# Kernel tuning notes

Hardware: AMD Instinct MI355X
Metric: run time of the kernel (lower is better)

## Reference

```python
import jax, jax.numpy as jnp
import numpy as np

N_NODES = 50000


def _graph_conv(x, src, dst, W, b):
    """DGL GraphConv with norm='both', bias, weight applied pre-aggregation.
    x: [N, Fin]; src/dst: [E] int; W: [Fin, Fout]; b: [Fout]."""
    N = x.shape[0]
    ones = jnp.ones(src.shape, jnp.float32)
    deg_out = jnp.maximum(jax.ops.segment_sum(ones, src, num_segments=N), 1.0)
    deg_in = jnp.maximum(jax.ops.segment_sum(ones, dst, num_segments=N), 1.0)
    h = (x * jax.lax.rsqrt(deg_out)[:, None]) @ W          # [N, Fout]
    m = jax.ops.segment_sum(h[src], dst, num_segments=N)   # SpMM aggregate
    return m * jax.lax.rsqrt(deg_in)[:, None] + b


def setup_inputs() -> dict:
    key = jax.random.key(0)
    ks = jax.random.split(key, 12)
    N = N_NODES
    e_sizes = {"rsr": 3000000, "rtr": 1000000, "rur": 200000}
    inp = {"x": jax.random.normal(ks[0], (N, 32), jnp.float32)}
    for i, (name, E) in enumerate(e_sizes.items()):
        inp[f"src_{name}"] = jax.random.randint(ks[1 + 2 * i], (E,), 0, N, jnp.int64)
        inp[f"dst_{name}"] = jax.random.randint(ks[2 + 2 * i], (E,), 0, N, jnp.int64)
    inp["W1"] = jax.random.normal(ks[7], (3, 32, 16), jnp.float32) / np.sqrt(32.0)
    inp["b1"] = jnp.zeros((3, 16), jnp.float32)
    inp["W2"] = jax.random.normal(ks[8], (3, 16, 1), jnp.float32) / np.sqrt(16.0)
    inp["b2"] = jnp.zeros((3, 1), jnp.float32)
    return inp


def reference(x, src_rsr, dst_rsr, src_rtr, dst_rtr, src_rur, dst_rur, W1, b1, W2, b2):
    edges = [(src_rsr, dst_rsr), (src_rtr, dst_rtr), (src_rur, dst_rur)]
    # layer 1: HeteroGraphConv(sum over relations) -> relu
    h = sum(_graph_conv(x, s, d, W1[r], b1[r]) for r, (s, d) in enumerate(edges))
    h = jax.nn.relu(h)
    # layer 2 -> squeeze
    out = sum(_graph_conv(h, s, d, W2[r], b2[r]) for r, (s, d) in enumerate(edges))
    return out[:, 0]
```

## Files before the change

kernel.cpp:

```cpp
#include <hip/hip_runtime.h>

#define N_NODES 50000
#define FH 16
#define NBUK 782
#define BSHIFT 6
#define BSTRIDE 800
#define TILE 4096
#define NCH2 64
#define NRNG 8
#define RNGSZ 6250
#define C1CAP 4608

#define OFF_INVOUT   0u
#define OFF_INVIN    150000u
#define OFF_BUKCNT   300000u
#define OFF_BSTART   302400u
#define OFF_GCUR     304800u
#define OFF_ROWPTR   307200u
#define OFF_HPROJ    457216u
#define OFF_AGGP     3657216u
#define OFF_SRCHIST  3657216u
#define OFF_HS       6057216u
#define OFF_PAIRS    6357216u
#define OFF_SRCSORT  10557216u

__global__ __launch_bounds__(256) void k_srcDeg(const int* s0, const int* s1, const int* s2,
                                                int E0, int E1, int E2,
                                                unsigned* __restrict__ histP,
                                                unsigned* __restrict__ bukCnt) {
    __shared__ unsigned bins[RNGSZ / 2];
    int c = blockIdx.x, rg = blockIdx.y, r = blockIdx.z;
    if (c == 0 && rg == 0 && r == 0) {
        for (int i = threadIdx.x; i < 3 * BSTRIDE; i += 256) bukCnt[i] = 0u;
    }
    const int* arr = (r == 0) ? s0 : (r == 1) ? s1 : s2;
    int E = (r == 0) ? E0 : (r == 1) ? E1 : E2;
    for (int i = threadIdx.x; i < RNGSZ / 2; i += 256) bins[i] = 0u;
    __syncthreads();
    int lo = rg * RNGSZ;
    int per = (((E + NCH2 - 1) / NCH2) + 7) & ~7;
    int a0 = c * per, a1 = min(a0 + per, E);
    for (int i = a0 + (int)threadIdx.x * 8; i < a1; i += 2048) {
        if (i + 8 <= a1) {
            int4 v1 = *reinterpret_cast<const int4*>(arr + i);
            int4 v2 = *reinterpret_cast<const int4*>(arr + i + 4);
            unsigned d0 = (unsigned)(v1.x - lo), d1 = (unsigned)(v1.y - lo);
            unsigned d2 = (unsigned)(v1.z - lo), d3 = (unsigned)(v1.w - lo);
            unsigned d4 = (unsigned)(v2.x - lo), d5 = (unsigned)(v2.y - lo);
            unsigned d6 = (unsigned)(v2.z - lo), d7 = (unsigned)(v2.w - lo);
            if (d0 < (unsigned)RNGSZ) atomicAdd(&bins[d0 >> 1], (d0 & 1u) ? 65536u : 1u);
            if (d1 < (unsigned)RNGSZ) atomicAdd(&bins[d1 >> 1], (d1 & 1u) ? 65536u : 1u);
            if (d2 < (unsigned)RNGSZ) atomicAdd(&bins[d2 >> 1], (d2 & 1u) ? 65536u : 1u);
            if (d3 < (unsigned)RNGSZ) atomicAdd(&bins[d3 >> 1], (d3 & 1u) ? 65536u : 1u);
            if (d4 < (unsigned)RNGSZ) atomicAdd(&bins[d4 >> 1], (d4 & 1u) ? 65536u : 1u);
            if (d5 < (unsigned)RNGSZ) atomicAdd(&bins[d5 >> 1], (d5 & 1u) ? 65536u : 1u);
            if (d6 < (unsigned)RNGSZ) atomicAdd(&bins[d6 >> 1], (d6 & 1u) ? 65536u : 1u);
            if (d7 < (unsigned)RNGSZ) atomicAdd(&bins[d7 >> 1], (d7 & 1u) ? 65536u : 1u);
        } else {
            for (int k2 = i; k2 < a1; k2++) {
                unsigned d = (unsigned)(arr[k2] - lo);
                if (d < (unsigned)RNGSZ) atomicAdd(&bins[d >> 1], (d & 1u) ? 65536u : 1u);
            }
        }
    }
    __syncthreads();
    unsigned* out = histP + ((size_t)r * NCH2 + c) * 25000 + rg * (RNGSZ / 2);
    for (int i = threadIdx.x; i < RNGSZ / 2; i += 256) out[i] = bins[i];
}

__global__ __launch_bounds__(256) void k_misc(const unsigned* __restrict__ histP,
                                              float* __restrict__ invOut,
                                              const int* d0p, const int* d1p, const int* d2p,
                                              int E0, int E1, int E2,
                                              unsigned* __restrict__ bukCnt) {
    __shared__ unsigned bins[NBUK];
    int r = blockIdx.y;
    if (blockIdx.x < 196) {
        int n = blockIdx.x * 256 + threadIdx.x;
        if (n >= N_NODES) return;
        const unsigned* p = histP + (size_t)r * NCH2 * 25000 + (n >> 1);
        unsigned s = 0;
#pragma unroll
        for (int c = 0; c < NCH2; c++) {
            unsigned w = p[(size_t)c * 25000];
            s += (n & 1) ? (w >> 16) : (w & 0xFFFFu);
        }
        invOut[r * N_NODES + n] = rsqrtf((float)(s ? s : 1u));
        return;
    }
    int c = blockIdx.x - 196;
    const int* arr = (r == 0) ? d0p : (r == 1) ? d1p : d2p;
    int E = (r == 0) ? E0 : (r == 1) ? E1 : E2;
    for (int i = threadIdx.x; i < NBUK; i += 256) bins[i] = 0u;
    __syncthreads();
    int per = (((E + 255) / 256) + 3) & ~3;
    int a0 = c * per, a1 = min(a0 + per, E);
    for (int i = a0 + (int)threadIdx.x * 4; i < a1; i += 1024) {
        if (i + 4 <= a1) {
            int4 v = *reinterpret_cast<const int4*>(arr + i);
            atomicAdd(&bins[((unsigned)v.x) >> BSHIFT], 1u);
            atomicAdd(&bins[((unsigned)v.y) >> BSHIFT], 1u);
            atomicAdd(&bins[((unsigned)v.z) >> BSHIFT], 1u);
            atomicAdd(&bins[((unsigned)v.w) >> BSHIFT], 1u);
        } else {
            for (int k2 = i; k2 < a1; k2++)
                atomicAdd(&bins[((unsigned)arr[k2]) >> BSHIFT], 1u);
        }
    }
    __syncthreads();
    for (int b = threadIdx.x; b < NBUK; b += 256)
        if (bins[b]) atomicAdd(&bukCnt[r * BSTRIDE + b], bins[b]);
}

__global__ __launch_bounds__(256) void k_bucketScan(const unsigned* __restrict__ bukCnt,
                                                    unsigned* __restrict__ bstart,
                                                    unsigned* __restrict__ gcur) {
    __shared__ unsigned part[256];
    int r = blockIdx.x, t = threadIdx.x;
    unsigned loc[4]; unsigned s = 0;
#pragma unroll
    for (int k = 0; k < 4; k++) {
        int idx = 4 * t + k;
        loc[k] = (idx < NBUK) ? bukCnt[r * BSTRIDE + idx] : 0u;
        s += loc[k];
    }
    part[t] = s;
    __syncthreads();
    for (int d = 1; d < 256; d <<= 1) {
        unsigned v = (t >= d) ? part[t - d] : 0u;
        __syncthreads();
        part[t] += v;
        __syncthreads();
    }
    unsigned run = part[t] - s;
#pragma unroll
    for (int k = 0; k < 4; k++) {
        int idx = 4 * t + k;
        if (idx <= NBUK) { bstart[r * BSTRIDE + idx] = run; gcur[r * BSTRIDE + idx] = run; }
        run += loc[k];
    }
}

__global__ __launch_bounds__(256) void k_passB(
    const int* s0p, const int* s1p, const int* s2p,
    const int* d0p, const int* d1p, const int* d2p,
    int E0, int E1, int E2, int po0, int po1, int po2,
    unsigned* __restrict__ pairsAll, unsigned* __restrict__ gcurAll) {
    __shared__ unsigned cnt[NBUK];
    __shared__ unsigned off[NBUK];
    __shared__ unsigned gbase[NBUK];
    __shared__ unsigned part[256];
    __shared__ unsigned spair[TILE];
    __shared__ unsigned saddr[TILE];
    int r = blockIdx.z;
    const int* src = (r == 0) ? s0p : (r == 1) ? s1p : s2p;
    const int* dst = (r == 0) ? d0p : (r == 1) ? d1p : d2p;
    int E = (r == 0) ? E0 : (r == 1) ? E1 : E2;
    unsigned* pairs = pairsAll + ((r == 0) ? po0 : (r == 1) ? po1 : po2);
    unsigned* gcur = gcurAll + r * BSTRIDE;
    int nb = gridDim.x;
    int chunk = (((E + nb - 1) / nb) + 15) & ~15;
    int c0 = blockIdx.x * chunk;
    int c1 = min(c0 + chunk, E);
    for (int t0 = c0; t0 < c1; t0 += TILE) {
        int tn = min(TILE, c1 - t0);
        for (int i = threadIdx.x; i < NBUK; i += 256) cnt[i] = 0u;
        __syncthreads();
        unsigned pk[16], bk[16], sl[16];
        if (tn == TILE) {
            int base = t0 + (int)threadIdx.x * 16;
#pragma unroll
            for (int q = 0; q < 4; q++) {
                int4 vs = *reinterpret_cast<const int4*>(src + base + q * 4);
                int4 vd = *reinterpret_cast<const int4*>(dst + base + q * 4);
                pk[q * 4 + 0] = ((unsigned)vd.x << 16) | (unsigned)vs.x;
                pk[q * 4 + 1] = ((unsigned)vd.y << 16) | (unsigned)vs.y;
                pk[q * 4 + 2] = ((unsigned)vd.z << 16) | (unsigned)vs.z;
                pk[q * 4 + 3] = ((unsigned)vd.w << 16) | (unsigned)vs.w;
                bk[q * 4 + 0] = (unsigned)vd.x >> BSHIFT;
                bk[q * 4 + 1] = (unsigned)vd.y >> BSHIFT;
                bk[q * 4 + 2] = (unsigned)vd.z >> BSHIFT;
                bk[q * 4 + 3] = (unsigned)vd.w >> BSHIFT;
            }
#pragma unroll
            for (int k = 0; k < 16; k++) sl[k] = atomicAdd(&cnt[bk[k]], 1u);
        } else {
#pragma unroll
            for (int k = 0; k < 16; k++) {
                int ii = k * 256 + (int)threadIdx.x;
                bk[k] = 0xFFFFFFFFu;
                if (ii < tn) {
                    int i = t0 + ii;
                    unsigned s = (unsigned)src[i], d = (unsigned)dst[i];
                    pk[k] = (d << 16) | s;
                    unsigned b = d >> BSHIFT;
                    bk[k] = b;
                    sl[k] = atomicAdd(&cnt[b], 1u);
                }
            }
        }
        __syncthreads();
        {
            int t = threadIdx.x;
            unsigned loc[4]; unsigned sloc = 0;
#pragma unroll
            for (int k2 = 0; k2 < 4; k2++) {
                int idx = 4 * t + k2;
                loc[k2] = (idx < NBUK) ? cnt[idx] : 0u;
                sloc += loc[k2];
            }
            part[t] = sloc;
            __syncthreads();
            for (int d = 1; d < 256; d <<= 1) {
                unsigned v = (t >= d) ? part[t - d] : 0u;
                __syncthreads();
                part[t] += v;
                __syncthreads();
            }
            unsigned run = part[t] - sloc;
#pragma unroll
            for (int k2 = 0; k2 < 4; k2++) {
                int idx = 4 * t + k2;
                if (idx < NBUK) off[idx] = run;
                run += loc[k2];
            }
        }
        __syncthreads();
        for (int b = threadIdx.x; b < NBUK; b += 256) {
            unsigned c = cnt[b];
            if (c) gbase[b] = atomicAdd(&gcur[b], c);
        }
        __syncthreads();
        if (tn == TILE) {
#pragma unroll
            for (int k = 0; k < 16; k++) {
                unsigned idx = off[bk[k]] + sl[k];
                spair[idx] = pk[k];
                saddr[idx] = gbase[bk[k]] + sl[k];
            }
        } else {
#pragma unroll
            for (int k = 0; k < 16; k++) {
                if (bk[k] != 0xFFFFFFFFu) {
                    unsigned idx = off[bk[k]] + sl[k];
                    spair[idx] = pk[k];
                    saddr[idx] = gbase[bk[k]] + sl[k];
                }
            }
        }
        __syncthreads();
#pragma unroll
        for (int k = 0; k < 16; k++) {
            int ii = k * 256 + (int)threadIdx.x;
            if (ii < tn) pairs[saddr[ii]] = spair[ii];
        }
        __syncthreads();
    }
}

__global__ __launch_bounds__(256) void k_h1(const float* __restrict__ x, const float* __restrict__ invOut,
                                            const float* __restrict__ W1, float* __restrict__ hproj) {
    __shared__ float sW[32 * FH];
    __shared__ float sx[16][32];
    int r = blockIdx.y;
    const float* W = W1 + r * 32 * FH;
    int t = threadIdx.x;
    for (int i = t; i < 32 * FH; i += 256) sW[i] = W[i];
    int n0 = blockIdx.x * 16;
    for (int i = t; i < 16 * 32; i += 256) {
        int nn = i >> 5, kk = i & 31;
        int n = n0 + nn;
        sx[nn][kk] = (n < N_NODES) ? x[n * 32 + kk] : 0.0f;
    }
    __syncthreads();
    int nn = t >> 4, j = t & 15;
    int n = n0 + nn;
    if (n < N_NODES) {
        float s = 0.f;
#pragma unroll
        for (int k = 0; k < 32; k++) s += sx[nn][k] * sW[k * FH + j];
        hproj[((size_t)r * N_NODES + n) * FH + j] = s * invOut[r * N_NODES + n];
    }
}

__global__ __launch_bounds__(256) void k_passC1(
    const unsigned* __restrict__ pairsAll, int po1, int po2,
    const unsigned* __restrict__ bstartAll,
    const float4* __restrict__ h4All, float4* __restrict__ out4All,
    unsigned short* __restrict__ srcGAll, unsigned* __restrict__ rowptrAll,
    float* __restrict__ invInAll) {
    __shared__ unsigned cnt[64];
    __shared__ unsigned off[65];
    __shared__ unsigned cur[64];
    __shared__ unsigned short srcS[C1CAP];
    int b = blockIdx.x, t = threadIdx.x, r = blockIdx.z;
    int po = (r == 0) ? 0 : (r == 1) ? po1 : po2;
    const unsigned* pairs = pairsAll + po;
    const unsigned* bstart = bstartAll + r * BSTRIDE;
    const float4* h4 = h4All + (size_t)r * N_NODES * 4;
    float4* out4 = out4All + (size_t)r * N_NODES * 4;
    unsigned short* srcG = srcGAll + po;
    unsigned* rowptr = rowptrAll + (size_t)r * (N_NODES + 1);
    float* invIn = invInAll + (size_t)r * N_NODES;
    unsigned e0 = bstart[b], e1 = bstart[b + 1];
    if (e1 - e0 > (unsigned)C1CAP) e1 = e0 + (unsigned)C1CAP;
    int d0 = b << BSHIFT;
    if (t < 64) cnt[t] = 0u;
    __syncthreads();
    for (unsigned i = e0 + t; i < e1; i += 256)
        atomicAdd(&cnt[(pairs[i] >> 16) - (unsigned)d0], 1u);
    __syncthreads();
    if (t < 64) {
        unsigned cv = cnt[t];
        unsigned sc = cv;
#pragma unroll
        for (int d = 1; d < 64; d <<= 1) {
            unsigned v = __shfl_up(sc, d, 64);
            if (t >= d) sc += v;
        }
        off[t] = sc - cv;
        if (t == 63) off[64] = sc;
    }
    __syncthreads();
    if (t < 64) {
        cur[t] = off[t];
        int n = d0 + t;
        if (n < N_NODES) {
            rowptr[n] = (unsigned)po + e0 + off[t];
            unsigned dg = cnt[t];
            invIn[n] = rsqrtf((float)(dg ? dg : 1u));
        }
    }
    if (b == NBUK - 1 && t == 0) rowptr[N_NODES] = (unsigned)po + e1;
    __syncthreads();
    for (unsigned i = e0 + t; i < e1; i += 256) {
        unsigned p = pairs[i];
        unsigned d = (p >> 16) - (unsigned)d0;
        unsigned pos = atomicAdd(&cur[d], 1u);
        srcS[pos] = (unsigned short)(p & 0xFFFFu);
    }
    __syncthreads();
    {
        unsigned len = e1 - e0;
        for (unsigned i = t; i < len; i += 256) srcG[e0 + i] = srcS[i];
    }
    int unit = t >> 4, p = t & 15, k = p >> 2, fq = p & 3;
    for (int nd = unit; nd < 64; nd += 16) {
        unsigned o0 = off[nd], o1 = off[nd + 1];
        float ax = 0.f, ay = 0.f, az = 0.f, aw = 0.f;
        unsigned base = o0;
        for (; base + 8 <= o1; base += 8) {
            int s0 = srcS[base + k], s1 = srcS[base + 4 + k];
            float4 v0 = h4[(size_t)s0 * 4 + fq];
            float4 v1 = h4[(size_t)s1 * 4 + fq];
            ax += v0.x + v1.x; ay += v0.y + v1.y; az += v0.z + v1.z; aw += v0.w + v1.w;
        }
        for (; base < o1; base += 4) {
            unsigned idx = base + (unsigned)k;
            if (idx < o1) {
                int s = srcS[idx];
                float4 v = h4[(size_t)s * 4 + fq];
                ax += v.x; ay += v.y; az += v.z; aw += v.w;
            }
        }
        ax += __shfl_xor(ax, 4, 16); ay += __shfl_xor(ay, 4, 16);
        az += __shfl_xor(az, 4, 16); aw += __shfl_xor(aw, 4, 16);
        ax += __shfl_xor(ax, 8, 16); ay += __shfl_xor(ay, 8, 16);
        az += __shfl_xor(az, 8, 16); aw += __shfl_xor(aw, 8, 16);
        int n = d0 + nd;
        if (k == 0 && n < N_NODES) {
            unsigned dg = o1 - o0;
            float sc = rsqrtf((float)(dg ? dg : 1u));
            float4 res; res.x = ax * sc; res.y = ay * sc; res.z = az * sc; res.w = aw * sc;
            out4[(size_t)n * 4 + fq] = res;
        }
    }
}

__global__ __launch_bounds__(256) void k_relu_h2(const float4* __restrict__ aggP4,
                                                 const float* __restrict__ invOut,
                                                 const float* __restrict__ b1,
                                                 const float* __restrict__ W2,
                                                 float* __restrict__ hs) {
    __shared__ float sW[3 * FH];
    __shared__ float sb[FH];
    int t = threadIdx.x;
    if (t < 48) sW[t] = W2[t];
    if (t < 16) sb[t] = b1[t] + b1[FH + t] + b1[2 * FH + t];
    __syncthreads();
    int n = blockIdx.x * 256 + t;
    if (n >= N_NODES) return;
    const size_t SL4 = (size_t)N_NODES * 4;
    float h[FH];
#pragma unroll
    for (int q = 0; q < 4; q++) {
        float4 a0 = aggP4[(size_t)n * 4 + q];
        float4 a1 = aggP4[SL4 + (size_t)n * 4 + q];
        float4 a2 = aggP4[2 * SL4 + (size_t)n * 4 + q];
        h[q * 4 + 0] = fmaxf(a0.x + a1.x + a2.x + sb[q * 4 + 0], 0.f);
        h[q * 4 + 1] = fmaxf(a0.y + a1.y + a2.y + sb[q * 4 + 1], 0.f);
        h[q * 4 + 2] = fmaxf(a0.z + a1.z + a2.z + sb[q * 4 + 2], 0.f);
        h[q * 4 + 3] = fmaxf(a0.w + a1.w + a2.w + sb[q * 4 + 3], 0.f);
    }
#pragma unroll
    for (int r = 0; r < 3; r++) {
        float s = 0.f;
#pragma unroll
        for (int j = 0; j < FH; j++) s += h[j] * sW[r * FH + j];
        hs[r * N_NODES + n] = s * invOut[r * N_NODES + n];
    }
}

__global__ __launch_bounds__(256) void k_passC2f(
    const unsigned short* __restrict__ srcG, const unsigned* __restrict__ rowptr,
    const float* __restrict__ hsAll, const float* __restrict__ invIn,
    const float* __restrict__ b2, float* __restrict__ out) {
    int t = threadIdx.x;
    int unit = t >> 4, p = t & 15;
    int n = blockIdx.x * 16 + unit;
    if (n >= N_NODES) return;
    float tot = 0.f;
#pragma unroll
    for (int r = 0; r < 3; r++) {
        unsigned o0 = rowptr[r * (N_NODES + 1) + n];
        unsigned o1 = rowptr[r * (N_NODES + 1) + n + 1];
        const float* hs = hsAll + (size_t)r * N_NODES;
        float s = 0.f;
        for (unsigned i = o0 + (unsigned)p; i < o1; i += 16) s += hs[srcG[i]];
        tot += s * invIn[r * N_NODES + n];
    }
    tot += __shfl_xor(tot, 1, 16); tot += __shfl_xor(tot, 2, 16);
    tot += __shfl_xor(tot, 4, 16); tot += __shfl_xor(tot, 8, 16);
    if (p == 0) out[n] = tot + b2[0] + b2[1] + b2[2];
}


__global__ void f_zero(float* __restrict__ p, int n) {
    int i = blockIdx.x * blockDim.x + threadIdx.x;
    if (i < n) p[i] = 0.0f;
}
__global__ void f_deg(const int* __restrict__ src, const int* __restrict__ dst, int E,
                      float* __restrict__ dout, float* __restrict__ din) {
    int i = blockIdx.x * blockDim.x + threadIdx.x;
    if (i < E) { atomicAdd(&dout[src[i]], 1.0f); atomicAdd(&din[dst[i]], 1.0f); }
}
__global__ void f_rsqrt(float* __restrict__ p, int n) {
    int i = blockIdx.x * blockDim.x + threadIdx.x;
    if (i < n) p[i] = rsqrtf(fmaxf(p[i], 1.0f));
}
__global__ void f_agg1(const int* __restrict__ src, const int* __restrict__ dst, int E,
                       const float* __restrict__ h, const float* __restrict__ invin,
                       float* __restrict__ agg) {
    int idx = blockIdx.x * blockDim.x + threadIdx.x;
    if (idx < E * FH) {
        int e = idx >> 4, j = idx & 15;
        atomicAdd(&agg[dst[e] * FH + j], h[src[e] * FH + j] * invin[dst[e]]);
    }
}
__global__ void f_relu(float* __restrict__ agg, const float* __restrict__ b1) {
    int i = blockIdx.x * blockDim.x + threadIdx.x;
    if (i < N_NODES * FH) {
        int j = i & 15;
        agg[i] = fmaxf(agg[i] + b1[j] + b1[FH + j] + b1[2 * FH + j], 0.0f);
    }
}
__global__ void f_outinit(float* __restrict__ out, const float* __restrict__ b2) {
    int i = blockIdx.x * blockDim.x + threadIdx.x;
    if (i < N_NODES) out[i] = b2[0] + b2[1] + b2[2];
}
__global__ void f_h2(const float* __restrict__ h1, const float* __restrict__ invout,
                     const float* __restrict__ W2r, float* __restrict__ hsv) {
    int n = blockIdx.x * blockDim.x + threadIdx.x;
    if (n < N_NODES) {
        const float4* hp = (const float4*)(h1 + (size_t)n * FH);
        float s = 0.0f;
#pragma unroll
        for (int q = 0; q < 4; q++) {
            float4 hv = hp[q];
            s += hv.x * W2r[q * 4] + hv.y * W2r[q * 4 + 1] + hv.z * W2r[q * 4 + 2] + hv.w * W2r[q * 4 + 3];
        }
        hsv[n] = s * invout[n];
    }
}
__global__ void f_agg2(const int* __restrict__ src, const int* __restrict__ dst, int E,
                       const float* __restrict__ hsv, const float* __restrict__ invin,
                       float* __restrict__ out) {
    int e = blockIdx.x * blockDim.x + threadIdx.x;
    if (e < E) atomicAdd(&out[dst[e]], hsv[src[e]] * invin[dst[e]]);
}


extern "C" void kernel_launch(void* const* d_in, const int* in_sizes, int n_in,
                              void* d_out, int out_size, void* d_ws, size_t ws_size,
                              hipStream_t stream) {
    const float* x = (const float*)d_in[0];
    const int* srcs[3] = { (const int*)d_in[1], (const int*)d_in[3], (const int*)d_in[5] };
    const int* dsts[3] = { (const int*)d_in[2], (const int*)d_in[4], (const int*)d_in[6] };
    int E[3] = { in_sizes[1], in_sizes[3], in_sizes[5] };
    const float* W1 = (const float*)d_in[7];
    const float* b1 = (const float*)d_in[8];
    const float* W2 = (const float*)d_in[9];
    const float* b2 = (const float*)d_in[10];
    float* out = (float*)d_out;
    const int N = N_NODES;
    const int B = 256;
    size_t Etot = (size_t)E[0] + E[1] + E[2];
    size_t need = ((size_t)OFF_SRCSORT + (Etot + 1) / 2) * 4u;

    if (ws_size >= need) {
        unsigned* ws = (unsigned*)d_ws;
        float* invOut = (float*)(ws + OFF_INVOUT);
        float* invIn  = (float*)(ws + OFF_INVIN);
        unsigned* bukCnt = ws + OFF_BUKCNT;
        unsigned* bstart = ws + OFF_BSTART;
        unsigned* gcur   = ws + OFF_GCUR;
        unsigned* rowptr = ws + OFF_ROWPTR;
        float* hproj = (float*)(ws + OFF_HPROJ);
        float* aggP  = (float*)(ws + OFF_AGGP);
        unsigned* srcHist = ws + OFF_SRCHIST;
        float* hs    = (float*)(ws + OFF_HS);
        unsigned* pairs = ws + OFF_PAIRS;
        unsigned short* srcSort = (unsigned short*)(ws + OFF_SRCSORT);
        int po[3] = { 0, E[0], E[0] + E[1] };

        k_srcDeg<<<dim3(NCH2, NRNG, 3), B, 0, stream>>>(srcs[0], srcs[1], srcs[2],
                                                        E[0], E[1], E[2], srcHist, bukCnt);
        k_misc<<<dim3(196 + 256, 3), B, 0, stream>>>(srcHist, invOut,
                                                     dsts[0], dsts[1], dsts[2],
                                                     E[0], E[1], E[2], bukCnt);
        k_bucketScan<<<3, B, 0, stream>>>(bukCnt, bstart, gcur);
        k_passB<<<dim3(256, 1, 3), B, 0, stream>>>(
            srcs[0], srcs[1], srcs[2], dsts[0], dsts[1], dsts[2],
            E[0], E[1], E[2], po[0], po[1], po[2], pairs, gcur);
        k_h1<<<dim3((N + 15) / 16, 3), B, 0, stream>>>(x, invOut, W1, hproj);
        k_passC1<<<dim3(NBUK, 1, 3), B, 0, stream>>>(
            pairs, po[1], po[2], bstart,
            (const float4*)hproj, (float4*)aggP,
            srcSort, rowptr, invIn);
        k_relu_h2<<<(N + B - 1) / B, B, 0, stream>>>((const float4*)aggP, invOut, b1, W2, hs);
        k_passC2f<<<(N + 15) / 16, B, 0, stream>>>(srcSort, rowptr, hs, invIn, b2, out);
    } else {
        float* wsf = (float*)d_ws;
        float* invOut = wsf;
        float* invIn = wsf + 3 * (size_t)N;
        float* h = wsf + 6 * (size_t)N;
        float* agg = wsf + 22 * (size_t)N;
        float* hsv = wsf + 38 * (size_t)N;
        f_zero<<<(6 * N + B - 1) / B, B, 0, stream>>>(invOut, 6 * N);
        f_zero<<<(16 * N + B - 1) / B, B, 0, stream>>>(agg, 16 * N);
        for (int r = 0; r < 3; r++)
            f_deg<<<(E[r] + B - 1) / B, B, 0, stream>>>(srcs[r], dsts[r], E[r],
                                                        invOut + (size_t)r * N, invIn + (size_t)r * N);
        f_rsqrt<<<(6 * N + B - 1) / B, B, 0, stream>>>(invOut, 6 * N);
        for (int r = 0; r < 3; r++) {
            k_h1<<<dim3((N + 15) / 16, 1), B, 0, stream>>>(x, invOut + (size_t)r * N,
                                                           W1 + (size_t)r * 32 * FH, h);
            f_agg1<<<(E[r] * FH + B - 1) / B, B, 0, stream>>>(srcs[r], dsts[r], E[r], h,
                                                              invIn + (size_t)r * N, agg);
        }
        f_relu<<<(N * FH + B - 1) / B, B, 0, stream>>>(agg, b1);
        f_outinit<<<(N + B - 1) / B, B, 0, stream>>>(out, b2);
        for (int r = 0; r < 3; r++) {
            f_h2<<<(N + B - 1) / B, B, 0, stream>>>(agg, invOut + (size_t)r * N,
                                                    W2 + (size_t)r * FH, hsv);
            f_agg2<<<(E[r] + B - 1) / B, B, 0, stream>>>(srcs[r], dsts[r], E[r], hsv,
                                                         invIn + (size_t)r * N, out);
        }
    }
}
```

Before: 242.6 us.

## Merge preprocessing kernels to cut launches and drop global bucket atomics

Fuses the source-degree and destination-bucket histograms into one launch, writing per-chunk bucket counts instead of using global atomics. Degree reduction and the bucket scan share one kernel that sums the partial counts. The partition pass and the layer-1 projection share a launch as disjoint block ranges. Together these go from six launches to three and let independent work fill the GPU together. The cost is extra partial-count memory and a serial 32-way sum per bucket in the scan block.

Result: slower. 247.7 us (+2.1%).

```diff
diff --git a/kernel.cpp b/kernel.cpp
--- a/kernel.cpp
+++ b/kernel.cpp
@@ -9,91 +9,73 @@
 #define NCH2 64
 #define NRNG 8
 #define RNGSZ 6250
+#define NDCH 32
 #define C1CAP 4608
 
 #define OFF_INVOUT   0u
 #define OFF_INVIN    150000u
-#define OFF_BUKCNT   300000u
 #define OFF_BSTART   302400u
 #define OFF_GCUR     304800u
 #define OFF_ROWPTR   307200u
 #define OFF_HPROJ    457216u
 #define OFF_AGGP     3657216u
 #define OFF_SRCHIST  3657216u
+#define OFF_BUKCNTP  8457216u
 #define OFF_HS       6057216u
 #define OFF_PAIRS    6357216u
 #define OFF_SRCSORT  10557216u
 
-__global__ __launch_bounds__(256) void k_srcDeg(const int* s0, const int* s1, const int* s2,
-                                                int E0, int E1, int E2,
-                                                unsigned* __restrict__ histP,
-                                                unsigned* __restrict__ bukCnt) {
+__global__ __launch_bounds__(256) void k_hist(
+    const int* s0, const int* s1, const int* s2,
+    const int* d0p, const int* d1p, const int* d2p,
+    int E0, int E1, int E2,
+    unsigned* __restrict__ histP, unsigned* __restrict__ bukCntP) {
     __shared__ unsigned bins[RNGSZ / 2];
-    int c = blockIdx.x, rg = blockIdx.y, r = blockIdx.z;
-    if (c == 0 && rg == 0 && r == 0) {
-        for (int i = threadIdx.x; i < 3 * BSTRIDE; i += 256) bukCnt[i] = 0u;
-    }
-    const int* arr = (r == 0) ? s0 : (r == 1) ? s1 : s2;
-    int E = (r == 0) ? E0 : (r == 1) ? E1 : E2;
-    for (int i = threadIdx.x; i < RNGSZ / 2; i += 256) bins[i] = 0u;
-    __syncthreads();
-    int lo = rg * RNGSZ;
-    int per = (((E + NCH2 - 1) / NCH2) + 7) & ~7;
-    int a0 = c * per, a1 = min(a0 + per, E);
-    for (int i = a0 + (int)threadIdx.x * 8; i < a1; i += 2048) {
-        if (i + 8 <= a1) {
-            int4 v1 = *reinterpret_cast<const int4*>(arr + i);
-            int4 v2 = *reinterpret_cast<const int4*>(arr + i + 4);
-            unsigned d0 = (unsigned)(v1.x - lo), d1 = (unsigned)(v1.y - lo);
-            unsigned d2 = (unsigned)(v1.z - lo), d3 = (unsigned)(v1.w - lo);
-            unsigned d4 = (unsigned)(v2.x - lo), d5 = (unsigned)(v2.y - lo);
-            unsigned d6 = (unsigned)(v2.z - lo), d7 = (unsigned)(v2.w - lo);
-            if (d0 < (unsigned)RNGSZ) atomicAdd(&bins[d0 >> 1], (d0 & 1u) ? 65536u : 1u);
-            if (d1 < (unsigned)RNGSZ) atomicAdd(&bins[d1 >> 1], (d1 & 1u) ? 65536u : 1u);
-            if (d2 < (unsigned)RNGSZ) atomicAdd(&bins[d2 >> 1], (d2 & 1u) ? 65536u : 1u);
-            if (d3 < (unsigned)RNGSZ) atomicAdd(&bins[d3 >> 1], (d3 & 1u) ? 65536u : 1u);
-            if (d4 < (unsigned)RNGSZ) atomicAdd(&bins[d4 >> 1], (d4 & 1u) ? 65536u : 1u);
-            if (d5 < (unsigned)RNGSZ) atomicAdd(&bins[d5 >> 1], (d5 & 1u) ? 65536u : 1u);
-            if (d6 < (unsigned)RNGSZ) atomicAdd(&bins[d6 >> 1], (d6 & 1u) ? 65536u : 1u);
-            if (d7 < (unsigned)RNGSZ) atomicAdd(&bins[d7 >> 1], (d7 & 1u) ? 65536u : 1u);
-        } else {
-            for (int k2 = i; k2 < a1; k2++) {
-                unsigned d = (unsigned)(arr[k2] - lo);
-                if (d < (unsigned)RNGSZ) atomicAdd(&bins[d >> 1], (d & 1u) ? 65536u : 1u);
-            }
-        }
-    }
-    __syncthreads();
-    unsigned* out = histP + ((size_t)r * NCH2 + c) * 25000 + rg * (RNGSZ / 2);
-    for (int i = threadIdx.x; i < RNGSZ / 2; i += 256) out[i] = bins[i];
-}
-
-__global__ __launch_bounds__(256) void k_misc(const unsigned* __restrict__ histP,
-                                              float* __restrict__ invOut,
-                                              const int* d0p, const int* d1p, const int* d2p,
-                                              int E0, int E1, int E2,
-                                              unsigned* __restrict__ bukCnt) {
-    __shared__ unsigned bins[NBUK];
-    int r = blockIdx.y;
-    if (blockIdx.x < 196) {
-        int n = blockIdx.x * 256 + threadIdx.x;
-        if (n >= N_NODES) return;
-        const unsigned* p = histP + (size_t)r * NCH2 * 25000 + (n >> 1);
-        unsigned s = 0;
-#pragma unroll
-        for (int c = 0; c < NCH2; c++) {
-            unsigned w = p[(size_t)c * 25000];
-            s += (n & 1) ? (w >> 16) : (w & 0xFFFFu);
-        }
-        invOut[r * N_NODES + n] = rsqrtf((float)(s ? s : 1u));
+    int bx = blockIdx.x;
+    if (bx < NCH2 * NRNG * 3) {
+        int c = bx % NCH2, rg = (bx / NCH2) % NRNG, r = bx / (NCH2 * NRNG);
+        const int* arr = (r == 0) ? s0 : (r == 1) ? s1 : s2;
+        int E = (r == 0) ? E0 : (r == 1) ? E1 : E2;
+        for (int i = threadIdx.x; i < RNGSZ / 2; i += 256) bins[i] = 0u;
+        __syncthreads();
+        int lo = rg * RNGSZ;
+        int per = (((E + NCH2 - 1) / NCH2) + 7) & ~7;
+        int a0 = c * per, a1 = min(a0 + per, E);
+        for (int i = a0 + (int)threadIdx.x * 8; i < a1; i += 2048) {
+            if (i + 8 <= a1) {
+                int4 v1 = *reinterpret_cast<const int4*>(arr + i);
+                int4 v2 = *reinterpret_cast<const int4*>(arr + i + 4);
+                unsigned d0 = (unsigned)(v1.x - lo), d1 = (unsigned)(v1.y - lo);
+                unsigned d2 = (unsigned)(v1.z - lo), d3 = (unsigned)(v1.w - lo);
+                unsigned d4 = (unsigned)(v2.x - lo), d5 = (unsigned)(v2.y - lo);
+                unsigned d6 = (unsigned)(v2.z - lo), d7 = (unsigned)(v2.w - lo);
+                if (d0 < (unsigned)RNGSZ) atomicAdd(&bins[d0 >> 1], (d0 & 1u) ? 65536u : 1u);
+                if (d1 < (unsigned)RNGSZ) atomicAdd(&bins[d1 >> 1], (d1 & 1u) ? 65536u : 1u);
+                if (d2 < (unsigned)RNGSZ) atomicAdd(&bins[d2 >> 1], (d2 & 1u) ? 65536u : 1u);
+                if (d3 < (unsigned)RNGSZ) atomicAdd(&bins[d3 >> 1], (d3 & 1u) ? 65536u : 1u);
+                if (d4 < (unsigned)RNGSZ) atomicAdd(&bins[d4 >> 1], (d4 & 1u) ? 65536u : 1u);
+                if (d5 < (unsigned)RNGSZ) atomicAdd(&bins[d5 >> 1], (d5 & 1u) ? 65536u : 1u);
+                if (d6 < (unsigned)RNGSZ) atomicAdd(&bins[d6 >> 1], (d6 & 1u) ? 65536u : 1u);
+                if (d7 < (unsigned)RNGSZ) atomicAdd(&bins[d7 >> 1], (d7 & 1u) ? 65536u : 1u);
+            } else {
+                for (int k2 = i; k2 < a1; k2++) {
+                    unsigned d = (unsigned)(arr[k2] - lo);
+                    if (d < (unsigned)RNGSZ) atomicAdd(&bins[d >> 1], (d & 1u) ? 65536u : 1u);
+                }
+            }
+        }
+        __syncthreads();
+        unsigned* out = histP + ((size_t)r * NCH2 + c) * 25000 + rg * (RNGSZ / 2);
+        for (int i = threadIdx.x; i < RNGSZ / 2; i += 256) out[i] = bins[i];
         return;
     }
-    int c = blockIdx.x - 196;
+    int idx = bx - NCH2 * NRNG * 3;
+    int c = idx % NDCH, r = idx / NDCH;
     const int* arr = (r == 0) ? d0p : (r == 1) ? d1p : d2p;
     int E = (r == 0) ? E0 : (r == 1) ? E1 : E2;
     for (int i = threadIdx.x; i < NBUK; i += 256) bins[i] = 0u;
     __syncthreads();
-    int per = (((E + 255) / 256) + 3) & ~3;
+    int per = (((E + NDCH - 1) / NDCH) + 3) & ~3;
     int a0 = c * per, a1 = min(a0 + per, E);
     for (int i = a0 + (int)threadIdx.x * 4; i < a1; i += 1024) {
         if (i + 4 <= a1) {
@@ -108,21 +90,41 @@
         }
     }
     __syncthreads();
-    for (int b = threadIdx.x; b < NBUK; b += 256)
-        if (bins[b]) atomicAdd(&bukCnt[r * BSTRIDE + b], bins[b]);
-}
-
-__global__ __launch_bounds__(256) void k_bucketScan(const unsigned* __restrict__ bukCnt,
-                                                    unsigned* __restrict__ bstart,
-                                                    unsigned* __restrict__ gcur) {
+    unsigned* outp = bukCntP + ((size_t)r * NDCH + c) * BSTRIDE;
+    for (int b = threadIdx.x; b < NBUK; b += 256) outp[b] = bins[b];
+}
+
+__global__ __launch_bounds__(256) void k_prep(const unsigned* __restrict__ histP,
+                                              float* __restrict__ invOut,
+                                              const unsigned* __restrict__ bukCntP,
+                                              unsigned* __restrict__ bstart,
+                                              unsigned* __restrict__ gcur) {
+    int r = blockIdx.y;
+    if (blockIdx.x < 196) {
+        int n = blockIdx.x * 256 + threadIdx.x;
+        if (n >= N_NODES) return;
+        const unsigned* p = histP + (size_t)r * NCH2 * 25000 + (n >> 1);
+        unsigned s = 0;
+#pragma unroll
+        for (int c = 0; c < NCH2; c++) {
+            unsigned w = p[(size_t)c * 25000];
+            s += (n & 1) ? (w >> 16) : (w & 0xFFFFu);
+        }
+        invOut[r * N_NODES + n] = rsqrtf((float)(s ? s : 1u));
+        return;
+    }
     __shared__ unsigned part[256];
-    int r = blockIdx.x, t = threadIdx.x;
+    int t = threadIdx.x;
     unsigned loc[4]; unsigned s = 0;
 #pragma unroll
     for (int k = 0; k < 4; k++) {
         int idx = 4 * t + k;
-        loc[k] = (idx < NBUK) ? bukCnt[r * BSTRIDE + idx] : 0u;
-        s += loc[k];
+        unsigned v = 0;
+        if (idx < NBUK) {
+            const unsigned* p = bukCntP + (size_t)r * NDCH * BSTRIDE + idx;
+            for (int c = 0; c < NDCH; c++) v += p[(size_t)c * BSTRIDE];
+        }
+        loc[k] = v; s += v;
     }
     part[t] = s;
     __syncthreads();
@@ -141,26 +143,55 @@
     }
 }
 
-__global__ __launch_bounds__(256) void k_passB(
+__global__ __launch_bounds__(256) void k_passB_h1(
     const int* s0p, const int* s1p, const int* s2p,
     const int* d0p, const int* d1p, const int* d2p,
     int E0, int E1, int E2, int po0, int po1, int po2,
-    unsigned* __restrict__ pairsAll, unsigned* __restrict__ gcurAll) {
-    __shared__ unsigned cnt[NBUK];
-    __shared__ unsigned off[NBUK];
-    __shared__ unsigned gbase[NBUK];
-    __shared__ unsigned part[256];
-    __shared__ unsigned spair[TILE];
-    __shared__ unsigned saddr[TILE];
-    int r = blockIdx.z;
+    unsigned* __restrict__ pairsAll, unsigned* __restrict__ gcurAll,
+    const float* __restrict__ x, const float* __restrict__ invOut,
+    const float* __restrict__ W1, float* __restrict__ hproj) {
+    __shared__ unsigned smem[NBUK * 3 + 256 + TILE * 2];
+    int bx = blockIdx.x;
+    if (bx >= 768) {
+        float* sW = (float*)smem;
+        float* sx = (float*)smem + 512;
+        int idx = bx - 768;
+        int r = idx / 3125;
+        int n0 = (idx - r * 3125) * 16;
+        const float* W = W1 + r * 32 * FH;
+        int t = threadIdx.x;
+        for (int i = t; i < 32 * FH; i += 256) sW[i] = W[i];
+        for (int i = t; i < 16 * 32; i += 256) {
+            int nn = i >> 5, kk = i & 31;
+            int n = n0 + nn;
+            sx[nn * 32 + kk] = (n < N_NODES) ? x[n * 32 + kk] : 0.0f;
+        }
+        __syncthreads();
+        int nn = t >> 4, j = t & 15;
+        int n = n0 + nn;
+        if (n < N_NODES) {
+            float s = 0.f;
+#pragma unroll
+            for (int k = 0; k < 32; k++) s += sx[nn * 32 + k] * sW[k * FH + j];
+            hproj[((size_t)r * N_NODES + n) * FH + j] = s * invOut[r * N_NODES + n];
+        }
+        return;
+    }
+    unsigned* cnt   = smem;
+    unsigned* off   = smem + NBUK;
+    unsigned* gbase = smem + 2 * NBUK;
+    unsigned* part  = smem + 3 * NBUK;
+    unsigned* spair = smem + 3 * NBUK + 256;
+    unsigned* saddr = spair + TILE;
+    int r = bx >> 8;
+    int cidx = bx & 255;
     const int* src = (r == 0) ? s0p : (r == 1) ? s1p : s2p;
     const int* dst = (r == 0) ? d0p : (r == 1) ? d1p : d2p;
     int E = (r == 0) ? E0 : (r == 1) ? E1 : E2;
     unsigned* pairs = pairsAll + ((r == 0) ? po0 : (r == 1) ? po1 : po2);
     unsigned* gcur = gcurAll + r * BSTRIDE;
-    int nb = gridDim.x;
-    int chunk = (((E + nb - 1) / nb) + 15) & ~15;
-    int c0 = blockIdx.x * chunk;
+    int chunk = (((E + 255) / 256) + 15) & ~15;
+    int c0 = cidx * chunk;
     int c1 = min(c0 + chunk, E);
     for (int t0 = c0; t0 < c1; t0 += TILE) {
         int tn = min(TILE, c1 - t0);
@@ -255,31 +286,6 @@
             if (ii < tn) pairs[saddr[ii]] = spair[ii];
         }
         __syncthreads();
-    }
-}
-
-__global__ __launch_bounds__(256) void k_h1(const float* __restrict__ x, const float* __restrict__ invOut,
-                                            const float* __restrict__ W1, float* __restrict__ hproj) {
-    __shared__ float sW[32 * FH];
-    __shared__ float sx[16][32];
-    int r = blockIdx.y;
-    const float* W = W1 + r * 32 * FH;
-    int t = threadIdx.x;
-    for (int i = t; i < 32 * FH; i += 256) sW[i] = W[i];
-    int n0 = blockIdx.x * 16;
-    for (int i = t; i < 16 * 32; i += 256) {
-        int nn = i >> 5, kk = i & 31;
-        int n = n0 + nn;
-        sx[nn][kk] = (n < N_NODES) ? x[n * 32 + kk] : 0.0f;
-    }
-    __syncthreads();
-    int nn = t >> 4, j = t & 15;
-    int n = n0 + nn;
-    if (n < N_NODES) {
-        float s = 0.f;
-#pragma unroll
-        for (int k = 0; k < 32; k++) s += sx[nn][k] * sW[k * FH + j];
-        hproj[((size_t)r * N_NODES + n) * FH + j] = s * invOut[r * N_NODES + n];
     }
 }
 
@@ -448,6 +454,28 @@
     int i = blockIdx.x * blockDim.x + threadIdx.x;
     if (i < n) p[i] = rsqrtf(fmaxf(p[i], 1.0f));
 }
+__global__ void f_h1(const float* __restrict__ x, const float* __restrict__ invout,
+                     const float* __restrict__ W, float* __restrict__ h) {
+    __shared__ float sW[32 * FH];
+    __shared__ float sx[16][32];
+    int t = threadIdx.x;
+    for (int i = t; i < 32 * FH; i += 256) sW[i] = W[i];
+    int n0 = blockIdx.x * 16;
+    for (int i = t; i < 16 * 32; i += 256) {
+        int nn = i >> 5, kk = i & 31;
+        int n = n0 + nn;
+        sx[nn][kk] = (n < N_NODES) ? x[n * 32 + kk] : 0.0f;
+    }
+    __syncthreads();
+    int nn = t >> 4, j = t & 15;
+    int n = n0 + nn;
+    if (n < N_NODES) {
+        float s = 0.f;
+#pragma unroll
+        for (int k = 0; k < 32; k++) s += sx[nn][k] * sW[k * FH + j];
+        h[n * FH + j] = s * invout[n];
+    }
+}
 __global__ void f_agg1(const int* __restrict__ src, const int* __restrict__ dst, int E,
                        const float* __restrict__ h, const float* __restrict__ invin,
                        float* __restrict__ agg) {
@@ -511,28 +539,26 @@
         unsigned* ws = (unsigned*)d_ws;
         float* invOut = (float*)(ws + OFF_INVOUT);
         float* invIn  = (float*)(ws + OFF_INVIN);
-        unsigned* bukCnt = ws + OFF_BUKCNT;
         unsigned* bstart = ws + OFF_BSTART;
         unsigned* gcur   = ws + OFF_GCUR;
         unsigned* rowptr = ws + OFF_ROWPTR;
         float* hproj = (float*)(ws + OFF_HPROJ);
         float* aggP  = (float*)(ws + OFF_AGGP);
         unsigned* srcHist = ws + OFF_SRCHIST;
+        unsigned* bukCntP = ws + OFF_BUKCNTP;
         float* hs    = (float*)(ws + OFF_HS);
         unsigned* pairs = ws + OFF_PAIRS;
         unsigned short* srcSort = (unsigned short*)(ws + OFF_SRCSORT);
         int po[3] = { 0, E[0], E[0] + E[1] };
 
-        k_srcDeg<<<dim3(NCH2, NRNG, 3), B, 0, stream>>>(srcs[0], srcs[1], srcs[2],
-                                                        E[0], E[1], E[2], srcHist, bukCnt);
-        k_misc<<<dim3(196 + 256, 3), B, 0, stream>>>(srcHist, invOut,
-                                                     dsts[0], dsts[1], dsts[2],
-                                                     E[0], E[1], E[2], bukCnt);
-        k_bucketScan<<<3, B, 0, stream>>>(bukCnt, bstart, gcur);
-        k_passB<<<dim3(256, 1, 3), B, 0, stream>>>(
+        k_hist<<<NCH2 * NRNG * 3 + NDCH * 3, B, 0, stream>>>(
             srcs[0], srcs[1], srcs[2], dsts[0], dsts[1], dsts[2],
-            E[0], E[1], E[2], po[0], po[1], po[2], pairs, gcur);
-        k_h1<<<dim3((N + 15) / 16, 3), B, 0, stream>>>(x, invOut, W1, hproj);
+            E[0], E[1], E[2], srcHist, bukCntP);
+        k_prep<<<dim3(197, 3), B, 0, stream>>>(srcHist, invOut, bukCntP, bstart, gcur);
+        k_passB_h1<<<768 + 3 * 3125, B, 0, stream>>>(
+            srcs[0], srcs[1], srcs[2], dsts[0], dsts[1], dsts[2],
+            E[0], E[1], E[2], po[0], po[1], po[2], pairs, gcur,
+            x, invOut, W1, hproj);
         k_passC1<<<dim3(NBUK, 1, 3), B, 0, stream>>>(
             pairs, po[1], po[2], bstart,
             (const float4*)hproj, (float4*)aggP,
@@ -553,8 +579,8 @@
                                                         invOut + (size_t)r * N, invIn + (size_t)r * N);
         f_rsqrt<<<(6 * N + B - 1) / B, B, 0, stream>>>(invOut, 6 * N);
         for (int r = 0; r < 3; r++) {
-            k_h1<<<dim3((N + 15) / 16, 1), B, 0, stream>>>(x, invOut + (size_t)r * N,
-                                                           W1 + (size_t)r * 32 * FH, h);
+            f_h1<<<(N + 15) / 16, B, 0, stream>>>(x, invOut + (size_t)r * N,
+                                                  W1 + (size_t)r * 32 * FH, h);
             f_agg1<<<(E[r] * FH + B - 1) / B, B, 0, stream>>>(srcs[r], dsts[r], E[r], h,
                                                               invIn + (size_t)r * N, agg);
         }
```
